# Performance work log

Hardware: AMD Instinct MI355X
Metric: run time of the kernel (lower is better)

## Reference

```python
import jax, jax.numpy as jnp
import numpy as np

B, Ci, Cr, Hb, Wb = 2, 256, 128, 200, 200
Ca, NH, DH = 128, 8, 16          # attn_channels = min(256,128); 8 heads of dim 16
K = 100                           # max(16, int(0.5*W)), K < W so topk path is active
EPS = 1e-5


def ln(x, g, b):
    m = x.mean(-1, keepdims=True)
    v = ((x - m) ** 2).mean(-1, keepdims=True)
    return (x - m) / jnp.sqrt(v + EPS) * g + b


def setup_inputs() -> dict:
    key = jax.random.key(0)
    ks = jax.random.split(key, 16)
    def n(k, shape, s=0.02):
        return jax.random.normal(k, shape, dtype=jnp.float32) * s
    return dict(
        radar_features=jax.random.normal(ks[0], (B, Cr, Hb, Wb), dtype=jnp.float32),
        image_features=jax.random.normal(ks[1], (B, Ci, Hb, Wb), dtype=jnp.float32),
        img_proj_w=n(ks[2], (Ca, Ci)),
        rad_proj_w=n(ks[3], (Ca, Cr)),
        in_proj_w=n(ks[4], (3 * Ca, Ca)),
        in_proj_b=jnp.zeros((3 * Ca,), jnp.float32),
        out_proj_w=n(ks[5], (Ca, Ca)),
        out_proj_b=jnp.zeros((Ca,), jnp.float32),
        ln1q_g=jnp.ones((Ca,), jnp.float32), ln1q_b=jnp.zeros((Ca,), jnp.float32),
        ln1kv_g=jnp.ones((Ca,), jnp.float32), ln1kv_b=jnp.zeros((Ca,), jnp.float32),
        ln2_g=jnp.ones((Ca,), jnp.float32), ln2_b=jnp.zeros((Ca,), jnp.float32),
        ffn_w1=n(ks[6], (4 * Ca, Ca)), ffn_b1=jnp.zeros((4 * Ca,), jnp.float32),
        ffn_w2=n(ks[7], (Ca, 4 * Ca)), ffn_b2=jnp.zeros((Ca,), jnp.float32),
        score_w1=n(ks[8], (Ca // 2, 2 * Ca)), score_b1=jnp.zeros((Ca // 2,), jnp.float32),
        score_w2=n(ks[9], (1, Ca // 2)), score_b2=jnp.zeros((1,), jnp.float32),
        rad_delta_w=n(ks[10], (Cr, Ca)),
        gamma=jnp.full((1,), 0.5, jnp.float32),  # torch inits to 0; 0.5 so attn branch affects output
        gate_w=n(ks[11], (Cr, Cr + Ci)), gate_b=jnp.zeros((Cr,), jnp.float32),
        fuse_w=n(ks[12], (Cr + Ci, Cr + Ci, 3, 3)),
        bn_g=jnp.ones((Cr + Ci,), jnp.float32), bn_b=jnp.zeros((Cr + Ci,), jnp.float32),
    )


def reference(radar_features, image_features, img_proj_w, rad_proj_w, in_proj_w, in_proj_b,
              out_proj_w, out_proj_b, ln1q_g, ln1q_b, ln1kv_g, ln1kv_b, ln2_g, ln2_b,
              ffn_w1, ffn_b1, ffn_w2, ffn_b2, score_w1, score_b1, score_w2, score_b2,
              rad_delta_w, gamma, gate_w, gate_b, fuse_w, bn_g, bn_b):
    # 1x1 projections into attention space, then per-row sequences [B*H, W, Ca]
    img_seq = jnp.einsum('bchw,oc->bhwo', image_features, img_proj_w).reshape(B * Hb, Wb, Ca)
    rad_seq = jnp.einsum('bchw,oc->bhwo', radar_features, rad_proj_w).reshape(B * Hb, Wb, Ca)

    # progressive focus: score each image token per row, keep top-K as KV
    si = jnp.concatenate([jax.lax.stop_gradient(rad_seq), img_seq], axis=-1)
    h = jax.nn.relu(si @ score_w1.T + score_b1)
    score = (h @ score_w2.T + score_b2)[..., 0]            # [B*H, W]
    _, idx = jax.lax.top_k(score, K)                       # [B*H, K]
    img_kv = jnp.take_along_axis(img_seq, idx[:, :, None], axis=1)  # [B*H, K, Ca]

    # cross attention (pre-LN on q and kv, residual onto rad_seq)
    q = ln(rad_seq, ln1q_g, ln1q_b)
    kv = ln(img_kv, ln1kv_g, ln1kv_b)
    wq, wk, wv = in_proj_w[:Ca], in_proj_w[Ca:2 * Ca], in_proj_w[2 * Ca:]
    bq, bk, bv = in_proj_b[:Ca], in_proj_b[Ca:2 * Ca], in_proj_b[2 * Ca:]
    qh = (q @ wq.T + bq).reshape(B * Hb, Wb, NH, DH)
    kh = (kv @ wk.T + bk).reshape(B * Hb, K, NH, DH)
    vh = (kv @ wv.T + bv).reshape(B * Hb, K, NH, DH)
    att = jax.nn.softmax(jnp.einsum('nqhd,nkhd->nhqk', qh, kh) / jnp.sqrt(jnp.float32(DH)), axis=-1)
    o = jnp.einsum('nhqk,nkhd->nqhd', att, vh).reshape(B * Hb, Wb, Ca) @ out_proj_w.T + out_proj_b
    x = rad_seq + o
    x = x + (jax.nn.relu(ln(x, ln2_g, ln2_b) @ ffn_w1.T + ffn_b1) @ ffn_w2.T + ffn_b2)

    # back to BEV, project delta to radar channels
    delta = jnp.einsum('bhwc,oc->bohw', x.reshape(B, Hb, Wb, Ca), rad_delta_w)

    # cross-modal gate (1x1 conv + sigmoid) with range-decay mask
    gate_in = jnp.concatenate([radar_features, image_features], axis=1)
    gate = jax.nn.sigmoid(jnp.einsum('bchw,oc->bohw', gate_in, gate_w) + gate_b[None, :, None, None])
    y = jnp.arange(Hb, dtype=jnp.float32) / (Hb - 1)
    rmask = jnp.clip(1.0 - 0.7 * y, 0.3, None)[None, None, :, None]
    gate = gate * rmask

    radar_enhanced = radar_features + gamma * gate * delta

    # fuse: 3x3 conv + BatchNorm (batch stats, training mode) + ReLU
    fi = jnp.concatenate([radar_enhanced, image_features], axis=1)
    c = jax.lax.conv_general_dilated(fi, fuse_w, (1, 1), 'SAME',
                                     dimension_numbers=('NCHW', 'OIHW', 'NCHW'))
    m = c.mean((0, 2, 3), keepdims=True)
    v = ((c - m) ** 2).mean((0, 2, 3), keepdims=True)
    out = jax.nn.relu((c - m) / jnp.sqrt(v + EPS) * bn_g[None, :, None, None] + bn_b[None, :, None, None])
    return out
```

## Files before the change

### kernel.cpp

```cpp
#include <hip/hip_runtime.h>
#include <hip/hip_bf16.h>

#define EPSF 1e-5f

typedef unsigned short u16;
typedef __attribute__((ext_vector_type(8))) short short8v;
typedef __attribute__((ext_vector_type(4))) float f32x4;

__device__ float g_arena[84000000];
__device__ float g_stats[768];

__device__ __forceinline__ float wave_sum(float v) {
#pragma unroll
    for (int o = 32; o > 0; o >>= 1) v += __shfl_down(v, o, 64);
    return v;
}

__device__ __forceinline__ float dot4(float4 a, float4 b) {
    return a.x * b.x + a.y * b.y + a.z * b.z + a.w * b.w;
}

__device__ __forceinline__ void bf_split(float v, u16& h, u16& l) {
    __hip_bfloat16 bh = __float2bfloat16(v);
    float hv = __bfloat162float(bh);
    __hip_bfloat16 bl = __float2bfloat16(v - hv);
    h = *reinterpret_cast<u16*>(&bh);
    l = *reinterpret_cast<u16*>(&bl);
}

__device__ __forceinline__ void store_split4(u16* ph, u16* pl, float4 v) {
    u16 h0, l0, h1, l1, h2, l2, h3, l3;
    bf_split(v.x, h0, l0); bf_split(v.y, h1, l1);
    bf_split(v.z, h2, l2); bf_split(v.w, h3, l3);
    *(ushort4*)ph = make_ushort4(h0, h1, h2, h3);
    *(ushort4*)pl = make_ushort4(l0, l1, l2, l3);
}

__global__ __launch_bounds__(256) void split_weights_kernel(
    const float* __restrict__ w_inproj, const float* __restrict__ w_outproj,
    const float* __restrict__ w_ffn1, const float* __restrict__ w_ffn2,
    const float* __restrict__ w_delta, const float* __restrict__ w_gate,
    const float* __restrict__ w_img, const float* __restrict__ w_rad,
    u16* __restrict__ wseg)
{
    int i = blockIdx.x * 256 + threadIdx.x;
    float v; int base, numel, local;
    if (i < 49152)       { local = i;          base = 0;      numel = 49152; v = w_inproj[local]; }
    else if (i < 65536)  { local = i - 49152;  base = 98304;  numel = 16384; v = w_outproj[local]; }
    else if (i < 131072) { local = i - 65536;  base = 131072; numel = 65536; v = w_ffn1[local]; }
    else if (i < 196608) { local = i - 131072; base = 262144; numel = 65536; v = w_ffn2[local]; }
    else if (i < 212992) { local = i - 196608; base = 393216; numel = 16384; v = w_delta[local]; }
    else if (i < 262144) { local = i - 212992; base = 425984; numel = 49152; v = w_gate[local]; }
    else {
        local = i - 262144; base = 524288; numel = 98304;
        int oc = local / 384, c = local - oc * 384;
        if (oc < 128) v = (c < 128) ? w_rad[oc * 128 + c] : 0.f;
        else          v = (c >= 128) ? w_img[(oc - 128) * 256 + (c - 128)] : 0.f;
    }
    u16 hh, ll;
    bf_split(v, hh, ll);
    wseg[base + local] = hh;
    wseg[base + numel + local] = ll;
}

template <int BMODE, int OMODE, bool RELU>
__global__ __launch_bounds__(256, 2) void mfma_gemm_kernel(
    const u16* __restrict__ Ah, const u16* __restrict__ Al,
    const u16* __restrict__ bh, const u16* __restrict__ bl,
    const float* __restrict__ bf, int bstride,
    const float* __restrict__ bias, const float* __restrict__ resid, int rstride,
    float* __restrict__ outf, u16* __restrict__ outh,
    int K, int Nout, int P)
{
    __shared__ alignas(16) u16 sAh[8192], sAl[8192], sBh[8192], sBl[8192];

    const int tid  = threadIdx.x;
    const int lane = tid & 63;
    const int wid  = tid >> 6;
    const int wrm  = wid >> 1;
    const int wcn  = wid & 1;
    const int ocb  = blockIdx.x * 128;
    const int p0   = blockIdx.y * 128;

    const int r0  = tid >> 3;
    const int cl  = tid & 7;
    const int swz = cl ^ (r0 & 7);

    f32x4 acc[4][4];
#pragma unroll
    for (int i = 0; i < 4; ++i)
#pragma unroll
        for (int j = 0; j < 4; ++j) acc[i][j] = (f32x4){0.f, 0.f, 0.f, 0.f};

    const int fr = lane & 15;
    const int fc = lane >> 4;

    for (int kk = 0; kk < K; kk += 64) {
        __syncthreads();
#pragma unroll
        for (int k = 0; k < 4; ++k) {
            int row = r0 + k * 32;
            int di = row * 64 + swz * 8;
            size_t ga = (size_t)(ocb + row) * K + kk + cl * 8;
            *(short8v*)&sAh[di] = *(const short8v*)&Ah[ga];
            *(short8v*)&sAl[di] = *(const short8v*)&Al[ga];
            int p = p0 + row;
            if (BMODE == 0) {
                if (p < P) {
                    size_t gb = (size_t)p * bstride + kk + cl * 8;
                    *(short8v*)&sBh[di] = *(const short8v*)&bh[gb];
                    *(short8v*)&sBl[di] = *(const short8v*)&bl[gb];
                } else {
                    short8v z = {0,0,0,0,0,0,0,0};
                    *(short8v*)&sBh[di] = z;
                    *(short8v*)&sBl[di] = z;
                }
            } else if (BMODE == 1) {
                if (p < P) {
                    size_t gb = (size_t)p * bstride + kk + cl * 8;
                    *(short8v*)&sBh[di] = *(const short8v*)&bh[gb];
                } else {
                    short8v z = {0,0,0,0,0,0,0,0};
                    *(short8v*)&sBh[di] = z;
                }
            } else {
                short8v vh8 = {0,0,0,0,0,0,0,0}, vl8 = {0,0,0,0,0,0,0,0};
                if (p < P) {
                    const float* src = bf + (size_t)p * bstride + kk + cl * 8;
                    float4 f0 = *(const float4*)(src);
                    float4 f1 = *(const float4*)(src + 4);
                    float fv[8] = {f0.x, f0.y, f0.z, f0.w, f1.x, f1.y, f1.z, f1.w};
#pragma unroll
                    for (int j = 0; j < 8; ++j) {
                        u16 hh, ll;
                        bf_split(fv[j], hh, ll);
                        vh8[j] = (short)hh;
                        vl8[j] = (short)ll;
                    }
                }
                *(short8v*)&sBh[di] = vh8;
                *(short8v*)&sBl[di] = vl8;
            }
        }
        __syncthreads();
#pragma unroll
        for (int h = 0; h < 2; ++h) {
            const int kc = h * 4 + fc;
            short8v bhf[4], blf[4];
#pragma unroll
            for (int nn = 0; nn < 4; ++nn) {
                int row = wcn * 64 + nn * 16 + fr;
                int idx = row * 64 + ((kc ^ (row & 7)) << 3);
                bhf[nn] = *(const short8v*)&sBh[idx];
                if (BMODE != 1) blf[nn] = *(const short8v*)&sBl[idx];
            }
#pragma unroll
            for (int mm = 0; mm < 4; ++mm) {
                int row = wrm * 64 + mm * 16 + fr;
                int idx = row * 64 + ((kc ^ (row & 7)) << 3);
                short8v ahf = *(const short8v*)&sAh[idx];
                short8v alf = *(const short8v*)&sAl[idx];
#pragma unroll
                for (int nn = 0; nn < 4; ++nn)
                    acc[mm][nn] = __builtin_amdgcn_mfma_f32_16x16x32_bf16(
                        ahf, bhf[nn], acc[mm][nn], 0, 0, 0);
                if (BMODE != 1) {
#pragma unroll
                    for (int nn = 0; nn < 4; ++nn)
                        acc[mm][nn] = __builtin_amdgcn_mfma_f32_16x16x32_bf16(
                            ahf, blf[nn], acc[mm][nn], 0, 0, 0);
                }
#pragma unroll
                for (int nn = 0; nn < 4; ++nn)
                    acc[mm][nn] = __builtin_amdgcn_mfma_f32_16x16x32_bf16(
                        alf, bhf[nn], acc[mm][nn], 0, 0, 0);
            }
        }
    }

#pragma unroll
    for (int mm = 0; mm < 4; ++mm) {
        int base = ocb + wrm * 64 + mm * 16 + fc * 4;
        float4 bv = {0.f, 0.f, 0.f, 0.f};
        if (bias) bv = *(const float4*)&bias[base];
#pragma unroll
        for (int nn = 0; nn < 4; ++nn) {
            int p = p0 + wcn * 64 + nn * 16 + fr;
            if (p < P) {
                size_t row = (size_t)p * Nout + base;
                float4 r;
                r.x = acc[mm][nn][0] + bv.x;
                r.y = acc[mm][nn][1] + bv.y;
                r.z = acc[mm][nn][2] + bv.z;
                r.w = acc[mm][nn][3] + bv.w;
                if (resid) {
                    float4 rr = *(const float4*)&resid[(size_t)p * rstride + base - ocb];
                    r.x += rr.x; r.y += rr.y; r.z += rr.z; r.w += rr.w;
                }
                if (RELU) {
                    r.x = fmaxf(r.x, 0.f); r.y = fmaxf(r.y, 0.f);
                    r.z = fmaxf(r.z, 0.f); r.w = fmaxf(r.w, 0.f);
                }
                if (OMODE == 0) {
                    *(float4*)&outf[row] = r;
                } else {
                    __hip_bfloat16 b0 = __float2bfloat16(r.x);
                    __hip_bfloat16 b1 = __float2bfloat16(r.y);
                    __hip_bfloat16 b2 = __float2bfloat16(r.z);
                    __hip_bfloat16 b3 = __float2bfloat16(r.w);
                    *(ushort4*)&outh[row] = make_ushort4(
                        *reinterpret_cast<u16*>(&b0), *reinterpret_cast<u16*>(&b1),
                        *reinterpret_cast<u16*>(&b2), *reinterpret_cast<u16*>(&b3));
                }
            }
        }
    }
}

__global__ __launch_bounds__(256) void score_kernel(
    const float* __restrict__ seq,
    const float* __restrict__ w1, const float* __restrict__ b1,
    const float* __restrict__ w2, const float* __restrict__ b2,
    float* __restrict__ score)
{
    __shared__ float sw1[64][20];
    __shared__ float ss[16][20];
    const int tid = threadIdx.x;
    const int p0 = blockIdx.x * 16;
    const int wvid = tid >> 6;
    const int l = tid & 63;
    float acc[4] = {0.f, 0.f, 0.f, 0.f};

    for (int cb = 0; cb < 256; cb += 16) {
        __syncthreads();
#pragma unroll
        for (int i = 0; i < 4; i++) {
            int e = tid + i * 256;
            int ll = e >> 4, cc = e & 15;
            sw1[ll][cc] = w1[(size_t)ll * 256 + cb + cc];
        }
        {
            int pos = tid >> 4, cc = tid & 15;
            ss[pos][cc] = seq[(size_t)(p0 + pos) * 256 + cb + cc];
        }
        __syncthreads();
#pragma unroll
        for (int c4 = 0; c4 < 4; c4++) {
            float4 wv = *(const float4*)&sw1[l][c4 * 4];
#pragma unroll
            for (int j = 0; j < 4; j++) {
                float4 sv = *(const float4*)&ss[wvid * 4 + j][c4 * 4];
                acc[j] += dot4(wv, sv);
            }
        }
    }
    float b1v = b1[l], w2v = w2[l], b2v = b2[0];
#pragma unroll
    for (int j = 0; j < 4; j++) {
        float h = fmaxf(acc[j] + b1v, 0.f);
        float v = wave_sum(h * w2v);
        if (l == 0) score[p0 + wvid * 4 + j] = v + b2v;
    }
}

__global__ __launch_bounds__(256) void topk_kernel(
    const float* __restrict__ score, int* __restrict__ idx)
{
    __shared__ float s[200];
    const int n = blockIdx.x;
    const int t = threadIdx.x;
    if (t < 200) s[t] = score[(size_t)n * 200 + t];
    __syncthreads();
    if (t < 200) {
        float my = s[t];
        int cnt = 0;
        for (int j = 0; j < 200; j++) {
            float o = s[j];
            cnt += (o > my) || (o == my && j < t);
        }
        if (cnt < 100) idx[n * 100 + cnt] = t;
    }
}

__global__ __launch_bounds__(256) void ln_gather_kernel(
    const float* __restrict__ in, int stride, const int* __restrict__ gidx,
    const float* __restrict__ g, const float* __restrict__ bb,
    u16* __restrict__ oh, u16* __restrict__ ol)
{
    __shared__ float red[4];
    const int tid = threadIdx.x;
    const int grp = tid >> 7;
    const int t = tid & 127;
    const int r = blockIdx.x * 2 + grp;

    size_t src_row;
    if (gidx) src_row = (size_t)(r / 100) * 200 + gidx[r];
    else      src_row = (size_t)r;

    float x = in[src_row * stride + t];
    float s = wave_sum(x);
    if ((tid & 63) == 0) red[tid >> 6] = s;
    __syncthreads();
    float m = (red[grp * 2] + red[grp * 2 + 1]) * 0.0078125f;
    float d = x - m;
    float s2 = wave_sum(d * d);
    __syncthreads();
    if ((tid & 63) == 0) red[tid >> 6] = s2;
    __syncthreads();
    float var = (red[grp * 2] + red[grp * 2 + 1]) * 0.0078125f;
    float y = d * rsqrtf(var + EPSF) * g[t] + bb[t];
    u16 hh, ll;
    bf_split(y, hh, ll);
    oh[(size_t)r * 128 + t] = hh;
    ol[(size_t)r * 128 + t] = ll;
}

__global__ __launch_bounds__(256) void attention_kernel(
    const float* __restrict__ qh, const float* __restrict__ kvh,
    u16* __restrict__ o_hi, u16* __restrict__ o_lo)
{
    __shared__ float sk[100][16];
    __shared__ float sv[100][16];
    const int h = blockIdx.x;
    const int n = blockIdx.y;
    const int tid = threadIdx.x;

    for (int e = tid; e < 1600; e += 256) {
        int kk = e >> 4, d = e & 15;
        size_t src = ((size_t)n * 100 + kk) * 256 + h * 16 + d;
        sk[kk][d] = kvh[src];
        sv[kk][d] = kvh[src + 128];
    }
    __syncthreads();

    if (tid < 200) {
        const float* qp = &qh[((size_t)n * 200 + tid) * 128 + h * 16];
        float4 q0 = *(const float4*)(qp + 0);
        float4 q1 = *(const float4*)(qp + 4);
        float4 q2 = *(const float4*)(qp + 8);
        float4 q3 = *(const float4*)(qp + 12);

        float m = -INFINITY, l = 0.f;
        float4 a0 = {0,0,0,0}, a1 = {0,0,0,0}, a2 = {0,0,0,0}, a3 = {0,0,0,0};

        for (int kk = 0; kk < 100; kk++) {
            const float4* kp = (const float4*)&sk[kk][0];
            float s = dot4(q0, kp[0]) + dot4(q1, kp[1]) +
                      dot4(q2, kp[2]) + dot4(q3, kp[3]);
            s *= 0.25f;
            float nm = fmaxf(m, s);
            float corr = __expf(m - nm);
            float pe = __expf(s - nm);
            l = l * corr + pe;
            const float4* vp = (const float4*)&sv[kk][0];
            float4 v0 = vp[0], v1 = vp[1], v2 = vp[2], v3 = vp[3];
            a0.x = a0.x * corr + pe * v0.x; a0.y = a0.y * corr + pe * v0.y;
            a0.z = a0.z * corr + pe * v0.z; a0.w = a0.w * corr + pe * v0.w;
            a1.x = a1.x * corr + pe * v1.x; a1.y = a1.y * corr + pe * v1.y;
            a1.z = a1.z * corr + pe * v1.z; a1.w = a1.w * corr + pe * v1.w;
            a2.x = a2.x * corr + pe * v2.x; a2.y = a2.y * corr + pe * v2.y;
            a2.z = a2.z * corr + pe * v2.z; a2.w = a2.w * corr + pe * v2.w;
            a3.x = a3.x * corr + pe * v3.x; a3.y = a3.y * corr + pe * v3.y;
            a3.z = a3.z * corr + pe * v3.z; a3.w = a3.w * corr + pe * v3.w;
            m = nm;
        }
        float inv = 1.f / l;
        a0.x *= inv; a0.y *= inv; a0.z *= inv; a0.w *= inv;
        a1.x *= inv; a1.y *= inv; a1.z *= inv; a1.w *= inv;
        a2.x *= inv; a2.y *= inv; a2.z *= inv; a2.w *= inv;
        a3.x *= inv; a3.y *= inv; a3.z *= inv; a3.w *= inv;
        size_t ob = ((size_t)n * 200 + tid) * 128 + h * 16;
        store_split4(&o_hi[ob + 0],  &o_lo[ob + 0],  a0);
        store_split4(&o_hi[ob + 4],  &o_lo[ob + 4],  a1);
        store_split4(&o_hi[ob + 8],  &o_lo[ob + 8],  a2);
        store_split4(&o_hi[ob + 12], &o_lo[ob + 12], a3);
    }
}

__global__ __launch_bounds__(256) void prep_weights_kernel(
    const float* __restrict__ fw, u16* __restrict__ wh, u16* __restrict__ wl)
{
    int idx = blockIdx.x * 256 + threadIdx.x;
    int oc = idx / 384;
    int ic = idx - oc * 384;
    const float* src = fw + (size_t)idx * 9;
    u16* dh = wh + (size_t)oc * 3456 + ic;
    u16* dl = wl + (size_t)oc * 3456 + ic;
#pragma unroll
    for (int s = 0; s < 9; ++s) {
        u16 hh, ll;
        bf_split(src[s], hh, ll);
        dh[(size_t)s * 384] = hh;
        dl[(size_t)s * 384] = ll;
    }
}

__global__ __launch_bounds__(256) void convert_nhwc_kernel(
    const float* __restrict__ radar, const float* __restrict__ image,
    u16* __restrict__ oh, u16* __restrict__ ol)
{
    int p = blockIdx.x * 256 + threadIdx.x;
    if (p >= 80000) return;
    int cg = blockIdx.y;
    int b = p >= 40000 ? 1 : 0;
    int hw = p - b * 40000;
    u16* ph = oh + (size_t)p * 384 + cg * 64;
    u16* pl = ol + (size_t)p * 384 + cg * 64;
#pragma unroll 1
    for (int g = 0; g < 8; ++g) {
        short8v vh, vl;
#pragma unroll
        for (int j = 0; j < 8; ++j) {
            int c = cg * 64 + g * 8 + j;
            float v = (c < 128)
                ? radar[((size_t)(b * 128 + c)) * 40000 + hw]
                : image[((size_t)(b * 256 + (c - 128))) * 40000 + hw];
            u16 hh, ll;
            bf_split(v, hh, ll);
            vh[j] = (short)hh;
            vl[j] = (short)ll;
        }
        *(short8v*)&ph[g * 8] = vh;
        *(short8v*)&pl[g * 8] = vl;
    }
}

__global__ __launch_bounds__(256) void enhance_fuse_kernel(
    const float* __restrict__ delta, const float* __restrict__ gatepre,
    const float* __restrict__ radar, const float* __restrict__ gamma_p,
    u16* __restrict__ nh)
{
    __shared__ float srad[64][136];
    const int tid = threadIdx.x;
    const int blk = blockIdx.x;
    const int b = blk >= 625 ? 1 : 0;
    const int hw0 = (blk - b * 625) * 64;
    const int p0 = b * 40000 + hw0;

#pragma unroll
    for (int i = 0; i < 32; ++i) {
        int e = tid + i * 256;
        int oc = e >> 6, pos = e & 63;
        srad[pos][oc] = radar[((size_t)(b * 128 + oc)) * 40000 + hw0 + pos];
    }
    __syncthreads();

    const float gmm = gamma_p[0];
    const int c4 = tid & 31;
    const int rr = tid >> 5;
#pragma unroll
    for (int j = 0; j < 8; ++j) {
        int pos = j * 8 + rr;
        int p = p0 + pos;
        int hw = hw0 + pos;
        int hrow = hw / 200;
        float rm = fmaxf(0.3f, 1.0f - 0.7f * ((float)hrow * (1.0f / 199.0f)));
        float4 dv = *(const float4*)&delta[(size_t)p * 128 + c4 * 4];
        float4 gv = *(const float4*)&gatepre[(size_t)p * 128 + c4 * 4];
        float4 rv = *(const float4*)&srad[pos][c4 * 4];
        float rx = rv.x + gmm * (1.f / (1.f + __expf(-gv.x))) * rm * dv.x;
        float ry = rv.y + gmm * (1.f / (1.f + __expf(-gv.y))) * rm * dv.y;
        float rz = rv.z + gmm * (1.f / (1.f + __expf(-gv.z))) * rm * dv.z;
        float rw = rv.w + gmm * (1.f / (1.f + __expf(-gv.w))) * rm * dv.w;
        __hip_bfloat16 b0 = __float2bfloat16(rx);
        __hip_bfloat16 b1 = __float2bfloat16(ry);
        __hip_bfloat16 b2 = __float2bfloat16(rz);
        __hip_bfloat16 b3 = __float2bfloat16(rw);
        *(ushort4*)&nh[(size_t)p * 384 + c4 * 4] = make_ushort4(
            *reinterpret_cast<u16*>(&b0), *reinterpret_cast<u16*>(&b1),
            *reinterpret_cast<u16*>(&b2), *reinterpret_cast<u16*>(&b3));
    }
}

__global__ __launch_bounds__(256, 3) void conv_mfma_kernel(
    const u16* __restrict__ nhwc_hi,
    const u16* __restrict__ wgt_hi,  const u16* __restrict__ wgt_lo,
    float* __restrict__ out)
{
    __shared__ alignas(16) u16 sAh[8192], sAl[8192], sBh[8192];

    const int tid  = threadIdx.x;
    const int lane = tid & 63;
    const int wid  = tid >> 6;
    const int wrm  = wid >> 1;
    const int wcn  = wid & 1;
    const int hw0  = blockIdx.x * 128;
    const int b    = blockIdx.y;
    const int oc0  = blockIdx.z * 128;

    const int r0  = tid >> 3;
    const int cl  = tid & 7;
    const int swz = cl ^ (r0 & 7);

    const int y0 = hw0 / 200;
    const int x0 = hw0 - y0 * 200;

    f32x4 acc[4][4];
#pragma unroll
    for (int i = 0; i < 4; ++i)
#pragma unroll
        for (int j = 0; j < 4; ++j) acc[i][j] = (f32x4){0.f, 0.f, 0.f, 0.f};

    size_t abase[4];
#pragma unroll
    for (int k = 0; k < 4; ++k)
        abase[k] = (size_t)(oc0 + r0 + k * 32) * 3456 + cl * 8;

    const int fr = lane & 15;
    const int fc = lane >> 4;

    for (int s = 0; s < 9; ++s) {
        const int dy = s / 3 - 1;
        const int dx = s % 3 - 1;
        size_t bsrc[4];
        int bval[4];
#pragma unroll
        for (int k = 0; k < 4; ++k) {
            int row = r0 + k * 32;
            int hwo = hw0 + row;
            int xr  = x0 + row;
            int wrp = (xr >= 200) ? 1 : 0;
            int yy  = y0 + wrp + dy;
            int xx  = xr - wrp * 200 + dx;
            int v = (hwo < 40000) && ((unsigned)yy < 200u) && ((unsigned)xx < 200u);
            bval[k] = v;
            bsrc[k] = v ? ((size_t)(b * 40000 + yy * 200 + xx) * 384 + cl * 8) : 0;
        }
        const size_t wofs = (size_t)s * 384;

        for (int icb = 0; icb < 6; ++icb) {
            const int ic0 = icb * 64;
            __syncthreads();
#pragma unroll
            for (int k = 0; k < 4; ++k) {
                int di = (r0 + k * 32) * 64 + swz * 8;
                size_t ga = abase[k] + wofs + ic0;
                *(short8v*)&sAh[di] = *(const short8v*)&wgt_hi[ga];
                *(short8v*)&sAl[di] = *(const short8v*)&wgt_lo[ga];
                if (bval[k]) {
                    *(short8v*)&sBh[di] = *(const short8v*)&nhwc_hi[bsrc[k] + ic0];
                } else {
                    short8v z = {0, 0, 0, 0, 0, 0, 0, 0};
                    *(short8v*)&sBh[di] = z;
                }
            }
            __syncthreads();
#pragma unroll
            for (int h = 0; h < 2; ++h) {
                const int kc = h * 4 + fc;
                short8v bhf[4];
#pragma unroll
                for (int nn = 0; nn < 4; ++nn) {
                    int row = wcn * 64 + nn * 16 + fr;
                    int idx = row * 64 + ((kc ^ (row & 7)) << 3);
                    bhf[nn] = *(const short8v*)&sBh[idx];
                }
#pragma unroll
                for (int mm = 0; mm < 4; ++mm) {
                    int row = wrm * 64 + mm * 16 + fr;
                    int idx = row * 64 + ((kc ^ (row & 7)) << 3);
                    short8v ahf = *(const short8v*)&sAh[idx];
                    short8v alf = *(const short8v*)&sAl[idx];
#pragma unroll
                    for (int nn = 0; nn < 4; ++nn)
                        acc[mm][nn] = __builtin_amdgcn_mfma_f32_16x16x32_bf16(
                            ahf, bhf[nn], acc[mm][nn], 0, 0, 0);
#pragma unroll
                    for (int nn = 0; nn < 4; ++nn)
                        acc[mm][nn] = __builtin_amdgcn_mfma_f32_16x16x32_bf16(
                            alf, bhf[nn], acc[mm][nn], 0, 0, 0);
                }
            }
        }
    }

#pragma unroll
    for (int mm = 0; mm < 4; ++mm) {
        int oc = oc0 + wrm * 64 + mm * 16 + fc * 4;
#pragma unroll
        for (int nn = 0; nn < 4; ++nn) {
            int p = hw0 + wcn * 64 + nn * 16 + fr;
            if (p < 40000) {
                float* op = out + (size_t)(b * 384 + oc) * 40000 + p;
#pragma unroll
                for (int r = 0; r < 4; ++r)
                    op[(size_t)r * 40000] = acc[mm][nn][r];
            }
        }
    }
}

__global__ __launch_bounds__(256) void conv_stats_kernel(const float* __restrict__ out)
{
    const int c = blockIdx.x;
    float s1 = 0.f, s2 = 0.f;
#pragma unroll
    for (int b = 0; b < 2; ++b) {
        const float4* pp = (const float4*)(out + (size_t)(b * 384 + c) * 40000);
        for (int i = threadIdx.x; i < 10000; i += 256) {
            float4 v = pp[i];
            s1 += v.x + v.y + v.z + v.w;
            s2 += v.x * v.x + v.y * v.y + v.z * v.z + v.w * v.w;
        }
    }
    s1 = wave_sum(s1);
    s2 = wave_sum(s2);
    __shared__ float r1[4], r2[4];
    if ((threadIdx.x & 63) == 0) {
        r1[threadIdx.x >> 6] = s1;
        r2[threadIdx.x >> 6] = s2;
    }
    __syncthreads();
    if (threadIdx.x == 0) {
        g_stats[c * 2]     = r1[0] + r1[1] + r1[2] + r1[3];
        g_stats[c * 2 + 1] = r2[0] + r2[1] + r2[2] + r2[3];
    }
}

__global__ __launch_bounds__(256) void bn_relu_kernel(
    float* __restrict__ out, const float* __restrict__ g,
    const float* __restrict__ bb)
{
    int i = blockIdx.x * 256 + threadIdx.x;
    int flat = i * 4;
    int oc = (flat / 40000) % 384;
    float m = g_stats[oc * 2] * (1.f / 80000.f);
    float v = g_stats[oc * 2 + 1] * (1.f / 80000.f) - m * m;
    float inv = rsqrtf(v + EPSF);
    float sc = g[oc] * inv;
    float sh = bb[oc] - m * sc;
    float4 c = ((float4*)out)[i];
    c.x = fmaxf(c.x * sc + sh, 0.f);
    c.y = fmaxf(c.y * sc + sh, 0.f);
    c.z = fmaxf(c.z * sc + sh, 0.f);
    c.w = fmaxf(c.w * sc + sh, 0.f);
    ((float4*)out)[i] = c;
}

extern "C" void kernel_launch(void* const* d_in, const int* in_sizes, int n_in,
                              void* d_out, int out_size, void* d_ws, size_t ws_size,
                              hipStream_t stream)
{
    (void)in_sizes; (void)n_in; (void)out_size; (void)d_ws; (void)ws_size;

    const float* radar      = (const float*)d_in[0];
    const float* image      = (const float*)d_in[1];
    const float* img_proj_w = (const float*)d_in[2];
    const float* rad_proj_w = (const float*)d_in[3];
    const float* in_proj_w  = (const float*)d_in[4];
    const float* in_proj_b  = (const float*)d_in[5];
    const float* out_proj_w = (const float*)d_in[6];
    const float* out_proj_b = (const float*)d_in[7];
    const float* ln1q_g     = (const float*)d_in[8];
    const float* ln1q_b     = (const float*)d_in[9];
    const float* ln1kv_g    = (const float*)d_in[10];
    const float* ln1kv_b    = (const float*)d_in[11];
    const float* ln2_g      = (const float*)d_in[12];
    const float* ln2_b      = (const float*)d_in[13];
    const float* ffn_w1     = (const float*)d_in[14];
    const float* ffn_b1     = (const float*)d_in[15];
    const float* ffn_w2     = (const float*)d_in[16];
    const float* ffn_b2     = (const float*)d_in[17];
    const float* score_w1   = (const float*)d_in[18];
    const float* score_b1   = (const float*)d_in[19];
    const float* score_w2   = (const float*)d_in[20];
    const float* score_b2   = (const float*)d_in[21];
    const float* rad_delta_w= (const float*)d_in[22];
    const float* gamma      = (const float*)d_in[23];
    const float* gate_w     = (const float*)d_in[24];
    const float* gate_b     = (const float*)d_in[25];
    const float* fuse_w     = (const float*)d_in[26];
    const float* bn_g       = (const float*)d_in[27];
    const float* bn_b       = (const float*)d_in[28];

    float* arena = nullptr;
    hipGetSymbolAddress((void**)&arena, HIP_SYMBOL(g_arena));

    u16*   nh_hi    = (u16*)arena;
    u16*   nh_lo    = (u16*)(arena + 15360000);
    float* seq_comb = arena + 30720000;
    float* score    = arena + 51200000;
    int*   idx      = (int*)(arena + 51280000);
    float* qh       = arena + 51200000;
    float* xbuf     = arena + 51200000;
    float* kvh      = arena + 61440000;
    float* gatepre  = arena + 61440000;
    u16*   gbase    = (u16*)(arena + 71680000);
    u16*   kvn_hi   = gbase,            *kvn_lo = gbase + 5120000;
    u16*   qn_hi    = gbase,            *qn_lo  = gbase + 10240000;
    u16*   o_hi     = gbase,            *o_lo   = gbase + 10240000;
    u16*   xn_hi    = gbase,            *xn_lo  = gbase + 10240000;
    float* delta    = arena + 71680000;
    u16*   hbuf     = (u16*)(arena + 30720000);
    u16*   wseg     = (u16*)(arena + 81920000);
    u16*   cwgt_hi  = (u16*)(arena + 82300000);
    u16*   cwgt_lo  = cwgt_hi + 1327104;

    const u16* w_q_hi    = wseg + 0,      *w_q_lo    = wseg + 49152;
    const u16* w_kv_hi   = wseg + 16384,  *w_kv_lo   = wseg + 49152 + 16384;
    const u16* w_out_hi  = wseg + 98304,  *w_out_lo  = wseg + 114688;
    const u16* w_ffn1_hi = wseg + 131072, *w_ffn1_lo = wseg + 196608;
    const u16* w_ffn2_hi = wseg + 262144, *w_ffn2_lo = wseg + 327680;
    const u16* w_dlt_hi  = wseg + 393216, *w_dlt_lo  = wseg + 409600;
    const u16* w_gate_hi = wseg + 425984, *w_gate_lo = wseg + 475136;
    const u16* w_comb_hi = wseg + 524288, *w_comb_lo = wseg + 622592;

    const dim3 blk(256);

    split_weights_kernel<<<dim3(1408), blk, 0, stream>>>(
        in_proj_w, out_proj_w, ffn_w1, ffn_w2, rad_delta_w, gate_w,
        img_proj_w, rad_proj_w, wseg);
    prep_weights_kernel<<<dim3(576), blk, 0, stream>>>(fuse_w, cwgt_hi, cwgt_lo);
    convert_nhwc_kernel<<<dim3(313, 6), blk, 0, stream>>>(radar, image, nh_hi, nh_lo);

    mfma_gemm_kernel<0, 0, false><<<dim3(2, 625), blk, 0, stream>>>(
        w_comb_hi, w_comb_lo, nh_hi, nh_lo, nullptr, 384,
        nullptr, nullptr, 0, seq_comb, nullptr, 384, 256, 80000);

    score_kernel<<<dim3(5000), blk, 0, stream>>>(
        seq_comb, score_w1, score_b1, score_w2, score_b2, score);
    topk_kernel<<<dim3(400), blk, 0, stream>>>(score, idx);

    ln_gather_kernel<<<dim3(20000), blk, 0, stream>>>(
        seq_comb + 128, 256, idx, ln1kv_g, ln1kv_b, kvn_hi, kvn_lo);
    mfma_gemm_kernel<0, 0, false><<<dim3(2, 313), blk, 0, stream>>>(
        w_kv_hi, w_kv_lo, kvn_hi, kvn_lo, nullptr, 128,
        in_proj_b + 128, nullptr, 0, kvh, nullptr, 128, 256, 40000);

    ln_gather_kernel<<<dim3(40000), blk, 0, stream>>>(
        seq_comb, 256, nullptr, ln1q_g, ln1q_b, qn_hi, qn_lo);
    mfma_gemm_kernel<0, 0, false><<<dim3(1, 625), blk, 0, stream>>>(
        w_q_hi, w_q_lo, qn_hi, qn_lo, nullptr, 128,
        in_proj_b, nullptr, 0, qh, nullptr, 128, 128, 80000);

    attention_kernel<<<dim3(8, 400), blk, 0, stream>>>(qh, kvh, o_hi, o_lo);

    mfma_gemm_kernel<0, 0, false><<<dim3(1, 625), blk, 0, stream>>>(
        w_out_hi, w_out_lo, o_hi, o_lo, nullptr, 128,
        out_proj_b, seq_comb, 256, xbuf, nullptr, 128, 128, 80000);

    ln_gather_kernel<<<dim3(40000), blk, 0, stream>>>(
        xbuf, 128, nullptr, ln2_g, ln2_b, xn_hi, xn_lo);
    mfma_gemm_kernel<0, 1, true><<<dim3(4, 625), blk, 0, stream>>>(
        w_ffn1_hi, w_ffn1_lo, xn_hi, xn_lo, nullptr, 128,
        ffn_b1, nullptr, 0, nullptr, hbuf, 128, 512, 80000);
    mfma_gemm_kernel<1, 0, false><<<dim3(1, 625), blk, 0, stream>>>(
        w_ffn2_hi, w_ffn2_lo, hbuf, nullptr, nullptr, 512,
        ffn_b2, xbuf, 128, xbuf, nullptr, 512, 128, 80000);

    mfma_gemm_kernel<2, 0, false><<<dim3(1, 625), blk, 0, stream>>>(
        w_dlt_hi, w_dlt_lo, nullptr, nullptr, xbuf, 128,
        nullptr, nullptr, 0, delta, nullptr, 128, 128, 80000);
    mfma_gemm_kernel<0, 0, false><<<dim3(1, 625), blk, 0, stream>>>(
        w_gate_hi, w_gate_lo, nh_hi, nh_lo, nullptr, 384,
        gate_b, nullptr, 0, gatepre, nullptr, 384, 128, 80000);
    enhance_fuse_kernel<<<dim3(1250), blk, 0, stream>>>(
        delta, gatepre, radar, gamma, nh_hi);

    conv_mfma_kernel<<<dim3(313, 2, 3), blk, 0, stream>>>(
        nh_hi, cwgt_hi, cwgt_lo, (float*)d_out);
    conv_stats_kernel<<<dim3(384), blk, 0, stream>>>((const float*)d_out);
    bn_relu_kernel<<<dim3(30000), blk, 0, stream>>>(
        (float*)d_out, bn_g, bn_b);
}
```

Baseline: 1.863 ms.

## Move score MLP to MFMA GEMM, reorder grids, split BN stats, drop gate lo input

The scalar score kernel is replaced by an MFMA GEMM with padded split-bf16 score weights and ReLU, followed by a small wave-reduction kernel for the second layer. The GEMM grid is transposed so consecutive blocks walk positions rather than output-channel tiles. The gate GEMM now reads only the high bf16 part of the activations, which drops some precision. Conv loops are reordered to iterate channel blocks outside the 3x3 taps, and BN statistics are split over four chunks per channel with atomics after a zeroing kernel, adding parallelism.

```diff
diff --git a/kernel.cpp b/kernel.cpp
--- a/kernel.cpp
+++ b/kernel.cpp
@@ -14,10 +14,6 @@
 #pragma unroll
     for (int o = 32; o > 0; o >>= 1) v += __shfl_down(v, o, 64);
     return v;
-}
-
-__device__ __forceinline__ float dot4(float4 a, float4 b) {
-    return a.x * b.x + a.y * b.y + a.z * b.z + a.w * b.w;
 }
 
 __device__ __forceinline__ void bf_split(float v, u16& h, u16& l) {
@@ -41,9 +37,16 @@
     const float* __restrict__ w_ffn1, const float* __restrict__ w_ffn2,
     const float* __restrict__ w_delta, const float* __restrict__ w_gate,
     const float* __restrict__ w_img, const float* __restrict__ w_rad,
-    u16* __restrict__ wseg)
+    const float* __restrict__ w_sc1, const float* __restrict__ b_sc1,
+    u16* __restrict__ wseg, float* __restrict__ bias_pad)
 {
     int i = blockIdx.x * 256 + threadIdx.x;
+    if (i >= 393344) return;
+    if (i >= 393216) {
+        int l = i - 393216;
+        bias_pad[l] = (l < 64) ? b_sc1[l] : 0.f;
+        return;
+    }
     float v; int base, numel, local;
     if (i < 49152)       { local = i;          base = 0;      numel = 49152; v = w_inproj[local]; }
     else if (i < 65536)  { local = i - 49152;  base = 98304;  numel = 16384; v = w_outproj[local]; }
@@ -51,11 +54,15 @@
     else if (i < 196608) { local = i - 131072; base = 262144; numel = 65536; v = w_ffn2[local]; }
     else if (i < 212992) { local = i - 196608; base = 393216; numel = 16384; v = w_delta[local]; }
     else if (i < 262144) { local = i - 212992; base = 425984; numel = 49152; v = w_gate[local]; }
-    else {
+    else if (i < 360448) {
         local = i - 262144; base = 524288; numel = 98304;
         int oc = local / 384, c = local - oc * 384;
         if (oc < 128) v = (c < 128) ? w_rad[oc * 128 + c] : 0.f;
         else          v = (c >= 128) ? w_img[(oc - 128) * 256 + (c - 128)] : 0.f;
+    } else {
+        local = i - 360448; base = 720896; numel = 32768;
+        int oc = local / 256, c = local - oc * 256;
+        v = (oc < 64) ? w_sc1[oc * 256 + c] : 0.f;
     }
     u16 hh, ll;
     bf_split(v, hh, ll);
@@ -79,8 +86,8 @@
     const int wid  = tid >> 6;
     const int wrm  = wid >> 1;
     const int wcn  = wid & 1;
-    const int ocb  = blockIdx.x * 128;
-    const int p0   = blockIdx.y * 128;
+    const int p0   = blockIdx.x * 128;
+    const int ocb  = blockIdx.y * 128;
 
     const int r0  = tid >> 3;
     const int cl  = tid & 7;
@@ -217,50 +224,15 @@
     }
 }
 
-__global__ __launch_bounds__(256) void score_kernel(
-    const float* __restrict__ seq,
-    const float* __restrict__ w1, const float* __restrict__ b1,
-    const float* __restrict__ w2, const float* __restrict__ b2,
-    float* __restrict__ score)
-{
-    __shared__ float sw1[64][20];
-    __shared__ float ss[16][20];
-    const int tid = threadIdx.x;
-    const int p0 = blockIdx.x * 16;
-    const int wvid = tid >> 6;
-    const int l = tid & 63;
-    float acc[4] = {0.f, 0.f, 0.f, 0.f};
-
-    for (int cb = 0; cb < 256; cb += 16) {
-        __syncthreads();
-#pragma unroll
-        for (int i = 0; i < 4; i++) {
-            int e = tid + i * 256;
-            int ll = e >> 4, cc = e & 15;
-            sw1[ll][cc] = w1[(size_t)ll * 256 + cb + cc];
-        }
-        {
-            int pos = tid >> 4, cc = tid & 15;
-            ss[pos][cc] = seq[(size_t)(p0 + pos) * 256 + cb + cc];
-        }
-        __syncthreads();
-#pragma unroll
-        for (int c4 = 0; c4 < 4; c4++) {
-            float4 wv = *(const float4*)&sw1[l][c4 * 4];
-#pragma unroll
-            for (int j = 0; j < 4; j++) {
-                float4 sv = *(const float4*)&ss[wvid * 4 + j][c4 * 4];
-                acc[j] += dot4(wv, sv);
-            }
-        }
-    }
-    float b1v = b1[l], w2v = w2[l], b2v = b2[0];
-#pragma unroll
-    for (int j = 0; j < 4; j++) {
-        float h = fmaxf(acc[j] + b1v, 0.f);
-        float v = wave_sum(h * w2v);
-        if (l == 0) score[p0 + wvid * 4 + j] = v + b2v;
-    }
+__global__ __launch_bounds__(256) void score_reduce_kernel(
+    const float* __restrict__ h, const float* __restrict__ w2,
+    const float* __restrict__ b2, float* __restrict__ score)
+{
+    int p = blockIdx.x * 4 + (threadIdx.x >> 6);
+    int l = threadIdx.x & 63;
+    float v = h[(size_t)p * 128 + l] * w2[l];
+    v = wave_sum(v);
+    if (l == 0) score[p] = v + b2[0];
 }
 
 __global__ __launch_bounds__(256) void topk_kernel(
@@ -345,8 +317,10 @@
 
         for (int kk = 0; kk < 100; kk++) {
             const float4* kp = (const float4*)&sk[kk][0];
-            float s = dot4(q0, kp[0]) + dot4(q1, kp[1]) +
-                      dot4(q2, kp[2]) + dot4(q3, kp[3]);
+            float s = q0.x*kp[0].x + q0.y*kp[0].y + q0.z*kp[0].z + q0.w*kp[0].w
+                    + q1.x*kp[1].x + q1.y*kp[1].y + q1.z*kp[1].z + q1.w*kp[1].w
+                    + q2.x*kp[2].x + q2.y*kp[2].y + q2.z*kp[2].z + q2.w*kp[2].w
+                    + q3.x*kp[3].x + q3.y*kp[3].y + q3.z*kp[3].z + q3.w*kp[3].w;
             s *= 0.25f;
             float nm = fmaxf(m, s);
             float corr = __expf(m - nm);
@@ -509,36 +483,36 @@
     const int fr = lane & 15;
     const int fc = lane >> 4;
 
-    for (int s = 0; s < 9; ++s) {
-        const int dy = s / 3 - 1;
-        const int dx = s % 3 - 1;
-        size_t bsrc[4];
-        int bval[4];
-#pragma unroll
-        for (int k = 0; k < 4; ++k) {
-            int row = r0 + k * 32;
-            int hwo = hw0 + row;
-            int xr  = x0 + row;
-            int wrp = (xr >= 200) ? 1 : 0;
-            int yy  = y0 + wrp + dy;
-            int xx  = xr - wrp * 200 + dx;
-            int v = (hwo < 40000) && ((unsigned)yy < 200u) && ((unsigned)xx < 200u);
-            bval[k] = v;
-            bsrc[k] = v ? ((size_t)(b * 40000 + yy * 200 + xx) * 384 + cl * 8) : 0;
-        }
-        const size_t wofs = (size_t)s * 384;
-
-        for (int icb = 0; icb < 6; ++icb) {
-            const int ic0 = icb * 64;
+    for (int icb = 0; icb < 6; ++icb) {
+        const int ic0 = icb * 64;
+        for (int s = 0; s < 9; ++s) {
+            const int dy = s / 3 - 1;
+            const int dx = s % 3 - 1;
+            size_t bsrc[4];
+            int bval[4];
+#pragma unroll
+            for (int k = 0; k < 4; ++k) {
+                int row = r0 + k * 32;
+                int hwo = hw0 + row;
+                int xr  = x0 + row;
+                int wrp = (xr >= 200) ? 1 : 0;
+                int yy  = y0 + wrp + dy;
+                int xx  = xr - wrp * 200 + dx;
+                int v = (hwo < 40000) && ((unsigned)yy < 200u) && ((unsigned)xx < 200u);
+                bval[k] = v;
+                bsrc[k] = v ? ((size_t)(b * 40000 + yy * 200 + xx) * 384 + cl * 8 + ic0) : 0;
+            }
+            const size_t wofs = (size_t)s * 384 + ic0;
+
             __syncthreads();
 #pragma unroll
             for (int k = 0; k < 4; ++k) {
                 int di = (r0 + k * 32) * 64 + swz * 8;
-                size_t ga = abase[k] + wofs + ic0;
+                size_t ga = abase[k] + wofs;
                 *(short8v*)&sAh[di] = *(const short8v*)&wgt_hi[ga];
                 *(short8v*)&sAl[di] = *(const short8v*)&wgt_lo[ga];
                 if (bval[k]) {
-                    *(short8v*)&sBh[di] = *(const short8v*)&nhwc_hi[bsrc[k] + ic0];
+                    *(short8v*)&sBh[di] = *(const short8v*)&nhwc_hi[bsrc[k]];
                 } else {
                     short8v z = {0, 0, 0, 0, 0, 0, 0, 0};
                     *(short8v*)&sBh[di] = z;
@@ -590,14 +564,21 @@
     }
 }
 
+__global__ void zero_stats_kernel() {
+    int i = blockIdx.x * 256 + threadIdx.x;
+    if (i < 768) g_stats[i] = 0.f;
+}
+
 __global__ __launch_bounds__(256) void conv_stats_kernel(const float* __restrict__ out)
 {
     const int c = blockIdx.x;
+    const int chunk = blockIdx.y;
     float s1 = 0.f, s2 = 0.f;
 #pragma unroll
     for (int b = 0; b < 2; ++b) {
-        const float4* pp = (const float4*)(out + (size_t)(b * 384 + c) * 40000);
-        for (int i = threadIdx.x; i < 10000; i += 256) {
+        const float4* pp = (const float4*)(out + (size_t)(b * 384 + c) * 40000)
+                         + (size_t)chunk * 2500;
+        for (int i = threadIdx.x; i < 2500; i += 256) {
             float4 v = pp[i];
             s1 += v.x + v.y + v.z + v.w;
             s2 += v.x * v.x + v.y * v.y + v.z * v.z + v.w * v.w;
@@ -612,8 +593,8 @@
     }
     __syncthreads();
     if (threadIdx.x == 0) {
-        g_stats[c * 2]     = r1[0] + r1[1] + r1[2] + r1[3];
-        g_stats[c * 2 + 1] = r2[0] + r2[1] + r2[2] + r2[3];
+        atomicAdd(&g_stats[c * 2],     r1[0] + r1[1] + r1[2] + r1[3]);
+        atomicAdd(&g_stats[c * 2 + 1], r2[0] + r2[1] + r2[2] + r2[3]);
     }
 }
 
@@ -685,6 +666,7 @@
     float* xbuf     = arena + 51200000;
     float* kvh      = arena + 61440000;
     float* gatepre  = arena + 61440000;
+    float* hscore   = arena + 71680000;
     u16*   gbase    = (u16*)(arena + 71680000);
     u16*   kvn_hi   = gbase,            *kvn_lo = gbase + 5120000;
     u16*   qn_hi    = gbase,            *qn_lo  = gbase + 10240000;
@@ -693,8 +675,9 @@
     float* delta    = arena + 71680000;
     u16*   hbuf     = (u16*)(arena + 30720000);
     u16*   wseg     = (u16*)(arena + 81920000);
-    u16*   cwgt_hi  = (u16*)(arena + 82300000);
+    u16*   cwgt_hi  = (u16*)(arena + 82330000);
     u16*   cwgt_lo  = cwgt_hi + 1327104;
+    float* bias_pad = arena + 83900000;
 
     const u16* w_q_hi    = wseg + 0,      *w_q_lo    = wseg + 49152;
     const u16* w_kv_hi   = wseg + 16384,  *w_kv_lo   = wseg + 49152 + 16384;
@@ -704,62 +687,67 @@
     const u16* w_dlt_hi  = wseg + 393216, *w_dlt_lo  = wseg + 409600;
     const u16* w_gate_hi = wseg + 425984, *w_gate_lo = wseg + 475136;
     const u16* w_comb_hi = wseg + 524288, *w_comb_lo = wseg + 622592;
+    const u16* w_sc1_hi  = wseg + 720896, *w_sc1_lo  = wseg + 753664;
 
     const dim3 blk(256);
 
-    split_weights_kernel<<<dim3(1408), blk, 0, stream>>>(
+    split_weights_kernel<<<dim3(1537), blk, 0, stream>>>(
         in_proj_w, out_proj_w, ffn_w1, ffn_w2, rad_delta_w, gate_w,
-        img_proj_w, rad_proj_w, wseg);
+        img_proj_w, rad_proj_w, score_w1, score_b1, wseg, bias_pad);
     prep_weights_kernel<<<dim3(576), blk, 0, stream>>>(fuse_w, cwgt_hi, cwgt_lo);
     convert_nhwc_kernel<<<dim3(313, 6), blk, 0, stream>>>(radar, image, nh_hi, nh_lo);
 
-    mfma_gemm_kernel<0, 0, false><<<dim3(2, 625), blk, 0, stream>>>(
+    mfma_gemm_kernel<0, 0, false><<<dim3(625, 2), blk, 0, stream>>>(
         w_comb_hi, w_comb_lo, nh_hi, nh_lo, nullptr, 384,
         nullptr, nullptr, 0, seq_comb, nullptr, 384, 256, 80000);
 
-    score_kernel<<<dim3(5000), blk, 0, stream>>>(
-        seq_comb, score_w1, score_b1, score_w2, score_b2, score);
+    mfma_gemm_kernel<2, 0, true><<<dim3(625, 1), blk, 0, stream>>>(
+        w_sc1_hi, w_sc1_lo, nullptr, nullptr, seq_comb, 256,
+        bias_pad, nullptr, 0, hscore, nullptr, 256, 128, 80000);
+    score_reduce_kernel<<<dim3(20000), blk, 0, stream>>>(
+        hscore, score_w2, score_b2, score);
     topk_kernel<<<dim3(400), blk, 0, stream>>>(score, idx);
 
     ln_gather_kernel<<<dim3(20000), blk, 0, stream>>>(
         seq_comb + 128, 256, idx, ln1kv_g, ln1kv_b, kvn_hi, kvn_lo);
-    mfma_gemm_kernel<0, 0, false><<<dim3(2, 313), blk, 0, stream>>>(
+    mfma_gemm_kernel<0, 0, false><<<dim3(313, 2), blk, 0, stream>>>(
         w_kv_hi, w_kv_lo, kvn_hi, kvn_lo, nullptr, 128,
         in_proj_b + 128, nullptr, 0, kvh, nullptr, 128, 256, 40000);
 
     ln_gather_kernel<<<dim3(40000), blk, 0, stream>>>(
         seq_comb, 256, nullptr, ln1q_g, ln1q_b, qn_hi, qn_lo);
-    mfma_gemm_kernel<0, 0, false><<<dim3(1, 625), blk, 0, stream>>>(
+    mfma_gemm_kernel<0, 0, false><<<dim3(625, 1), blk, 0, stream>>>(
         w_q_hi, w_q_lo, qn_hi, qn_lo, nullptr, 128,
         in_proj_b, nullptr, 0, qh, nullptr, 128, 128, 80000);
 
     attention_kernel<<<dim3(8, 400), blk, 0, stream>>>(qh, kvh, o_hi, o_lo);
 
-    mfma_gemm_kernel<0, 0, false><<<dim3(1, 625), blk, 0, stream>>>(
+    mfma_gemm_kernel<0, 0, false><<<dim3(625, 1), blk, 0, stream>>>(
         w_out_hi, w_out_lo, o_hi, o_lo, nullptr, 128,
         out_proj_b, seq_comb, 256, xbuf, nullptr, 128, 128, 80000);
 
     ln_gather_kernel<<<dim3(40000), blk, 0, stream>>>(
         xbuf, 128, nullptr, ln2_g, ln2_b, xn_hi, xn_lo);
-    mfma_gemm_kernel<0, 1, true><<<dim3(4, 625), blk, 0, stream>>>(
+    mfma_gemm_kernel<0, 1, true><<<dim3(625, 4), blk, 0, stream>>>(
         w_ffn1_hi, w_ffn1_lo, xn_hi, xn_lo, nullptr, 128,
         ffn_b1, nullptr, 0, nullptr, hbuf, 128, 512, 80000);
-    mfma_gemm_kernel<1, 0, false><<<dim3(1, 625), blk, 0, stream>>>(
+    mfma_gemm_kernel<1, 0, false><<<dim3(625, 1), blk, 0, stream>>>(
         w_ffn2_hi, w_ffn2_lo, hbuf, nullptr, nullptr, 512,
         ffn_b2, xbuf, 128, xbuf, nullptr, 512, 128, 80000);
 
-    mfma_gemm_kernel<2, 0, false><<<dim3(1, 625), blk, 0, stream>>>(
+    mfma_gemm_kernel<2, 0, false><<<dim3(625, 1), blk, 0, stream>>>(
         w_dlt_hi, w_dlt_lo, nullptr, nullptr, xbuf, 128,
         nullptr, nullptr, 0, delta, nullptr, 128, 128, 80000);
-    mfma_gemm_kernel<0, 0, false><<<dim3(1, 625), blk, 0, stream>>>(
-        w_gate_hi, w_gate_lo, nh_hi, nh_lo, nullptr, 384,
+    mfma_gemm_kernel<1, 0, false><<<dim3(625, 1), blk, 0, stream>>>(
+        w_gate_hi, w_gate_lo, nh_hi, nullptr, nullptr, 384,
         gate_b, nullptr, 0, gatepre, nullptr, 384, 128, 80000);
     enhance_fuse_kernel<<<dim3(1250), blk, 0, stream>>>(
         delta, gatepre, radar, gamma, nh_hi);
 
     conv_mfma_kernel<<<dim3(313, 2, 3), blk, 0, stream>>>(
         nh_hi, cwgt_hi, cwgt_lo, (float*)d_out);
-    conv_stats_kernel<<<dim3(384), blk, 0, stream>>>((const float*)d_out);
+    zero_stats_kernel<<<dim3(3), blk, 0, stream>>>();
+    conv_stats_kernel<<<dim3(384, 4), blk, 0, stream>>>((const float*)d_out);
     bn_relu_kernel<<<dim3(30000), blk, 0, stream>>>(
         (float*)d_out, bn_g, bn_b);
 }
```

New measurement: 2.160 ms. +16.0%, slower.
